# Optimization experiments

Hardware: AMD Instinct MI355X
Metric: run time of the kernel (lower is better)

Reference implementation:

```python
import jax, jax.numpy as jnp
import numpy as np

N, E = 50000, 800000
C_IN, C_OUT, HID = 64, 64, 64


def setup_inputs() -> dict:
    key = jax.random.key(0)
    ks = jax.random.split(key, 12)
    def rn(k, shape, scale=0.05):
        return jax.random.normal(k, shape, dtype=jnp.float32) * scale
    return dict(
        x=jax.random.normal(ks[0], (N, C_IN), dtype=jnp.float32),
        pos=jax.random.normal(ks[1], (N, 3), dtype=jnp.float32),
        edge_index=jax.random.randint(ks[2], (2, E), 0, N),
        W_in=rn(ks[3], (C_IN, C_IN)), b_in=jnp.zeros((C_IN,), jnp.float32),
        W_out=rn(ks[4], (C_OUT, C_OUT)), b_out=jnp.zeros((C_OUT,), jnp.float32),
        W_lin=rn(ks[5], (C_OUT, C_IN)),   # PointTransformerConv.lin (value), bias=False
        W_src=rn(ks[6], (C_OUT, C_IN)),   # lin_src, bias=False
        W_dst=rn(ks[7], (C_OUT, C_IN)),   # lin_dst, bias=False
        pos_w1=rn(ks[8], (HID, 3)), pos_b1=jnp.zeros((HID,), jnp.float32),
        pos_w2=rn(ks[9], (C_OUT, HID)), pos_b2=jnp.zeros((C_OUT,), jnp.float32),
        att_w1=rn(ks[10], (HID, C_OUT)), att_b1=jnp.zeros((HID,), jnp.float32),
        att_w2=rn(ks[11], (C_OUT, HID)), att_b2=jnp.zeros((C_OUT,), jnp.float32),
    )


def _mlp2(y, w1, b1, w2, b2):
    # MLP([a, 64, b], batch_norm=False): Linear->ReLU->Linear->ReLU
    y = jax.nn.relu(y @ w1.T + b1)
    return jax.nn.relu(y @ w2.T + b2)


def reference(x, pos, edge_index, W_in, b_in, W_out, b_out, W_lin, W_src, W_dst,
              pos_w1, pos_b1, pos_w2, pos_b2, att_w1, att_b1, att_w2, att_b2):
    n = x.shape[0]
    h = jax.nn.relu(x @ W_in.T + b_in)            # lin_in + relu, (N, C_in)
    v = h @ W_lin.T                                # value projection (N, C_out)
    k_src = h @ W_src.T                            # alpha_j source part
    q_dst = h @ W_dst.T                            # alpha_i dest part
    # PointTransformerConv adds self-loops by default
    loop = jnp.arange(n)
    src = jnp.concatenate([edge_index[0], loop])   # (E+N,)
    dst = jnp.concatenate([edge_index[1], loop])
    # per-edge positional encoding: pos_nn(pos_i - pos_j)
    delta = _mlp2(pos[dst] - pos[src], pos_w1, pos_b1, pos_w2, pos_b2)
    # per-edge attention logits: attn_nn(alpha_i - alpha_j), (E+N, C_out)
    alpha = _mlp2(q_dst[dst] - k_src[src], att_w1, att_b1, att_w2, att_b2)
    # per-destination-node channelwise softmax (self-loops ensure no empty segment)
    amax = jax.ops.segment_max(alpha, dst, num_segments=n)
    ex = jnp.exp(alpha - amax[dst])
    denom = jax.ops.segment_sum(ex, dst, num_segments=n)
    w = ex / (denom[dst] + 1e-16)
    # message = alpha * (x_j + delta); aggregate = sum over neighbors
    out = jax.ops.segment_sum(w * (v[src] + delta), dst, num_segments=n)
    return jax.nn.relu(out @ W_out.T + b_out)
```

## Files before the change

### kernel.cpp

```cpp
#include <hip/hip_runtime.h>
#include <math.h>

#define NN 50000
#define EE 800000
#define ET (EE + NN)
#define C  64
#define NBLK 49

typedef __attribute__((ext_vector_type(8))) _Float16 f16x8;
typedef __attribute__((ext_vector_type(4))) _Float16 f16x4;
typedef __attribute__((ext_vector_type(2))) _Float16 f16x2;
typedef __attribute__((ext_vector_type(4))) float f32x4;

__device__ __forceinline__ f16x2 pk2(float a, float b) {
  return __builtin_bit_cast(f16x2, __builtin_amdgcn_cvt_pkrtz(a, b));
}
__device__ __forceinline__ f16x4 pk4(float a, float b, float c, float d) {
  return __builtin_shufflevector(pk2(a, b), pk2(c, d), 0, 1, 2, 3);
}
__device__ __forceinline__ f16x8 pk8(const float* y) {
  const f16x4 lo = pk4(y[0], y[1], y[2], y[3]);
  const f16x4 hi = pk4(y[4], y[5], y[6], y[7]);
  return __builtin_shufflevector(lo, hi, 0, 1, 2, 3, 4, 5, 6, 7);
}

__device__ __forceinline__ f16x8 frag_ldh(const _Float16* base, int row,
                                          int kofs) {
  return *(const f16x8*)(base + row * 72 + kofs);
}

__device__ __forceinline__ void stage_w(_Float16* __restrict__ dst,
                                        const _Float16* __restrict__ src16,
                                        int tid) {
  const f16x8* src = (const f16x8*)(src16 + tid * 16);
  _Float16* d = dst + (tid >> 2) * 72 + (tid & 3) * 16;
  ((f16x8*)d)[0] = src[0];
  ((f16x8*)d)[1] = src[1];
}

__global__ __launch_bounds__(256) void prep_kernel(
    const float* __restrict__ W_in, const float* __restrict__ W_lin,
    const float* __restrict__ W_src, const float* __restrict__ W_dst,
    const float* __restrict__ att_w1, const float* __restrict__ att_w2,
    const float* __restrict__ pos_w2, const float* __restrict__ W_out,
    _Float16* __restrict__ w16) {
  const float* Ws[8] = {W_in, W_lin, W_src, W_dst, att_w1, att_w2, pos_w2, W_out};
  const float* src = Ws[blockIdx.x];
  _Float16* dst = w16 + blockIdx.x * 4096;
#pragma unroll
  for (int i = threadIdx.x * 4; i < 4096; i += 1024) {
    const float4 w = *(const float4*)(src + i);
    *(f16x4*)(dst + i) = pk4(w.x, w.y, w.z, w.w);
  }
}

__global__ __launch_bounds__(256) void scan_partial(const int* __restrict__ cnt,
                                                    int* __restrict__ bsum) {
  __shared__ int ws[4];
  const int t = threadIdx.x;
  const int base = blockIdx.x * 1024 + t * 4;
  int s = 0;
  if (base + 3 < NN) {
    const int4 v = *(const int4*)(cnt + base);
    s = v.x + v.y + v.z + v.w;
  } else {
#pragma unroll
    for (int i = 0; i < 4; ++i)
      if (base + i < NN) s += cnt[base + i];
  }
#pragma unroll
  for (int off = 32; off; off >>= 1) s += __shfl_down(s, off, 64);
  if ((t & 63) == 0) ws[t >> 6] = s;
  __syncthreads();
  if (t == 0) bsum[blockIdx.x] = ws[0] + ws[1] + ws[2] + ws[3];
}

__global__ __launch_bounds__(256) void scan_final(const int* __restrict__ cnt,
                                                  const int* __restrict__ bsum,
                                                  int* __restrict__ curs) {
  __shared__ int tsum[256];
  __shared__ int sblk[64];
  const int t = threadIdx.x;
  if (t < 64) {
    const int mine = (t < NBLK) ? bsum[t] : 0;
    int v = mine;
#pragma unroll
    for (int off = 1; off < 64; off <<= 1) {
      const int u = __shfl_up(v, off, 64);
      if (t >= off) v += u;
    }
    sblk[t] = v - mine;
  }
  const int base = blockIdx.x * 1024 + t * 4;
  int v[4] = {0, 0, 0, 0};
  if (base + 3 < NN) {
    const int4 x = *(const int4*)(cnt + base);
    v[0] = x.x; v[1] = x.y; v[2] = x.z; v[3] = x.w;
  } else {
#pragma unroll
    for (int i = 0; i < 4; ++i)
      if (base + i < NN) v[i] = cnt[base + i];
  }
  const int s = v[0] + v[1] + v[2] + v[3];
  tsum[t] = s;
  __syncthreads();
  for (int off = 1; off < 256; off <<= 1) {
    const int u = (t >= off) ? tsum[t - off] : 0;
    __syncthreads();
    tsum[t] += u;
    __syncthreads();
  }
  int ex = sblk[blockIdx.x] + tsum[t] - s;
#pragma unroll
  for (int i = 0; i < 4; ++i) {
    if (base + i < NN) curs[base + i] = ex;
    ex += v[i];
  }
}

__global__ void scatter_kernel(const int* __restrict__ ei,
                               int* __restrict__ curs, int2* __restrict__ srt) {
  const int e0 = (blockIdx.x * 256 + threadIdx.x) * 4;
  if (e0 >= ET) return;
  int s[4], d[4];
  if (e0 + 3 < EE) {
    const int4 sv = *(const int4*)(ei + e0);
    const int4 dv = *(const int4*)(ei + EE + e0);
    s[0] = sv.x; s[1] = sv.y; s[2] = sv.z; s[3] = sv.w;
    d[0] = dv.x; d[1] = dv.y; d[2] = dv.z; d[3] = dv.w;
  } else {
#pragma unroll
    for (int i = 0; i < 4; ++i) {
      const int e = e0 + i;
      if (e < EE) {
        s[i] = ei[e];
        d[i] = ei[EE + e];
      } else if (e < ET) {
        s[i] = d[i] = e - EE;
      } else {
        s[i] = d[i] = -1;
      }
    }
  }
#pragma unroll
  for (int i = 0; i < 4; ++i) {
    if (d[i] >= 0) {
      const int p = atomicAdd(&curs[d[i]], 1);
      srt[p] = make_int2(s[i], d[i]);
    }
  }
}

__global__ __launch_bounds__(256, 3) void node_proj(
    const float* __restrict__ x, const float* __restrict__ b_in,
    const _Float16* __restrict__ w16, const int* __restrict__ ei,
    int* __restrict__ cnt, _Float16* __restrict__ vh,
    _Float16* __restrict__ kh, _Float16* __restrict__ qh) {
  __shared__ __align__(16) _Float16 wlds[4 * 4608];
  __shared__ __align__(16) _Float16 hlds[4608];
  __shared__ float biasv[64];

  const int tid = threadIdx.x;
  const int nb = blockIdx.x * 64;
  const int l15 = tid & 15;
  const int quad = (tid >> 4) & 3;
  const int wband = tid >> 6;
  const int nloc = wband * 16 + l15;
  const int gn = nb + nloc;

  {
    const int stride = gridDim.x * 256;
    for (int e = blockIdx.x * 256 + tid; e < ET; e += stride) {
      const int d = (e < EE) ? ei[EE + e] : (e - EE);
      atomicAdd(&cnt[d], 1);
    }
  }

#pragma unroll
  for (int w = 0; w < 4; ++w) stage_w(wlds + w * 4608, w16 + w * 4096, tid);
  if (tid < 64) biasv[tid] = b_in[tid];

  f16x8 bfrag[2];
#pragma unroll
  for (int ks = 0; ks < 2; ++ks) {
    float y[8] = {0.f, 0.f, 0.f, 0.f, 0.f, 0.f, 0.f, 0.f};
    if (gn < NN) {
      const float4 a = *(const float4*)(x + (size_t)gn * 64 + ks * 32 + quad * 8);
      const float4 b = *(const float4*)(x + (size_t)gn * 64 + ks * 32 + quad * 8 + 4);
      y[0] = a.x; y[1] = a.y; y[2] = a.z; y[3] = a.w;
      y[4] = b.x; y[5] = b.y; y[6] = b.z; y[7] = b.w;
    }
    bfrag[ks] = pk8(y);
  }
  __syncthreads();

#pragma unroll
  for (int t = 0; t < 4; ++t) {
    f32x4 acc = {0.f, 0.f, 0.f, 0.f};
#pragma unroll
    for (int ks = 0; ks < 2; ++ks) {
      const f16x8 af = frag_ldh(wlds, t * 16 + l15, ks * 32 + quad * 8);
      acc = __builtin_amdgcn_mfma_f32_16x16x32_f16(af, bfrag[ks], acc, 0, 0, 0);
    }
    const int hb = t * 16 + quad * 4;
    *(f16x4*)(hlds + nloc * 72 + hb) =
        pk4(fmaxf(acc[0] + biasv[hb + 0], 0.f), fmaxf(acc[1] + biasv[hb + 1], 0.f),
            fmaxf(acc[2] + biasv[hb + 2], 0.f), fmaxf(acc[3] + biasv[hb + 3], 0.f));
  }
  __syncthreads();

  f16x8 hfrag[2];
#pragma unroll
  for (int ks = 0; ks < 2; ++ks)
    hfrag[ks] = frag_ldh(hlds, nloc, ks * 32 + quad * 8);

  _Float16* outs[3] = {vh, kh, qh};
#pragma unroll
  for (int p = 0; p < 3; ++p) {
    const _Float16* W = wlds + (p + 1) * 4608;
#pragma unroll
    for (int t = 0; t < 4; ++t) {
      f32x4 acc = {0.f, 0.f, 0.f, 0.f};
#pragma unroll
      for (int ks = 0; ks < 2; ++ks) {
        const f16x8 af = frag_ldh(W, t * 16 + l15, ks * 32 + quad * 8);
        acc = __builtin_amdgcn_mfma_f32_16x16x32_f16(af, hfrag[ks], acc, 0, 0, 0);
      }
      if (gn < NN) {
        *(f16x4*)(outs[p] + (size_t)gn * 64 + t * 16 + quad * 4) =
            pk4(acc[0], acc[1], acc[2], acc[3]);
      }
    }
  }
}

__global__ __launch_bounds__(256, 4) void edge_pass(
    const int2* __restrict__ srt, const float* __restrict__ pos,
    const _Float16* __restrict__ vh, const _Float16* __restrict__ kh,
    const _Float16* __restrict__ qh, const _Float16* __restrict__ w16,
    const float* __restrict__ att_b1, const float* __restrict__ att_b2,
    const float* __restrict__ pos_w1, const float* __restrict__ pos_b1,
    const float* __restrict__ pos_b2, float* __restrict__ num,
    float* __restrict__ den) {
  __shared__ __align__(16) _Float16 smem[18432];
  __shared__ __align__(16) float posw1T[3 * 64];
  __shared__ float b1s[64], b2s[64], pb1s[64], pb2s[64];
  __shared__ int dsts[64];

  _Float16* W1  = smem;
  _Float16* W2  = smem + 4608;
  _Float16* PW2 = smem + 9216;
  _Float16* h1  = smem + 13824;
  float2* pairb = (float2*)smem;

  const int tid = threadIdx.x;
  const int eb = blockIdx.x * 64;
  const int l15 = tid & 15;
  const int quad = (tid >> 4) & 3;
  const int wband = tid >> 6;
  const int eloc = wband * 16 + l15;

  int s_mine, d_mine;
  f16x8 bfrag[2];
  float dp0, dp1, dp2;
  {
    const int e = eb + eloc;
    int2 sd = make_int2(0, 0);
    int valid_d = -1;
    if (e < ET) {
      sd = srt[e];
      valid_d = sd.y;
    }
    s_mine = sd.x;
    d_mine = sd.y;
    if (quad == 0) dsts[eloc] = valid_d;
#pragma unroll
    for (int ks = 0; ks < 2; ++ks) {
      const f16x8 qv =
          *(const f16x8*)(qh + (size_t)d_mine * 64 + ks * 32 + quad * 8);
      const f16x8 kv =
          *(const f16x8*)(kh + (size_t)s_mine * 64 + ks * 32 + quad * 8);
      bfrag[ks] = qv - kv;
    }
    dp0 = pos[(size_t)d_mine * 3 + 0] - pos[(size_t)s_mine * 3 + 0];
    dp1 = pos[(size_t)d_mine * 3 + 1] - pos[(size_t)s_mine * 3 + 1];
    dp2 = pos[(size_t)d_mine * 3 + 2] - pos[(size_t)s_mine * 3 + 2];
  }

  stage_w(W1, w16 + 4 * 4096, tid);
  stage_w(W2, w16 + 5 * 4096, tid);
  stage_w(PW2, w16 + 6 * 4096, tid);
  if (tid < 64) {
    b1s[tid] = att_b1[tid];
    b2s[tid] = att_b2[tid];
    pb1s[tid] = pos_b1[tid];
    pb2s[tid] = pos_b2[tid];
    posw1T[0 * 64 + tid] = pos_w1[tid * 3 + 0];
    posw1T[1 * 64 + tid] = pos_w1[tid * 3 + 1];
    posw1T[2 * 64 + tid] = pos_w1[tid * 3 + 2];
  }
  __syncthreads();

#pragma unroll
  for (int t = 0; t < 4; ++t) {
    f32x4 acc = {0.f, 0.f, 0.f, 0.f};
#pragma unroll
    for (int ks = 0; ks < 2; ++ks) {
      const f16x8 af = frag_ldh(W1, t * 16 + l15, ks * 32 + quad * 8);
      acc = __builtin_amdgcn_mfma_f32_16x16x32_f16(af, bfrag[ks], acc, 0, 0, 0);
    }
    const int hb = t * 16 + quad * 4;
    *(f16x4*)(h1 + eloc * 72 + hb) =
        pk4(fmaxf(acc[0] + b1s[hb + 0], 0.f), fmaxf(acc[1] + b1s[hb + 1], 0.f),
            fmaxf(acc[2] + b1s[hb + 2], 0.f), fmaxf(acc[3] + b1s[hb + 3], 0.f));
  }

  f16x8 hpfrag[2];
#pragma unroll
  for (int ks = 0; ks < 2; ++ks) {
    float hv[8];
#pragma unroll
    for (int j = 0; j < 8; ++j) {
      const int i = ks * 32 + quad * 8 + j;
      float a = pb1s[i];
      a = fmaf(dp0, posw1T[i], a);
      a = fmaf(dp1, posw1T[64 + i], a);
      a = fmaf(dp2, posw1T[128 + i], a);
      hv[j] = fmaxf(a, 0.f);
    }
    hpfrag[ks] = pk8(hv);
  }
  __syncthreads();

  float ex[16], del[16];
  {
    f16x8 hfrag[2];
#pragma unroll
    for (int ks = 0; ks < 2; ++ks)
      hfrag[ks] = frag_ldh(h1, eloc, ks * 32 + quad * 8);
#pragma unroll
    for (int t = 0; t < 4; ++t) {
      f32x4 acc = {0.f, 0.f, 0.f, 0.f};
#pragma unroll
      for (int ks = 0; ks < 2; ++ks) {
        const f16x8 af = frag_ldh(W2, t * 16 + l15, ks * 32 + quad * 8);
        acc = __builtin_amdgcn_mfma_f32_16x16x32_f16(af, hfrag[ks], acc, 0, 0, 0);
      }
      const int ob = t * 16 + quad * 4;
#pragma unroll
      for (int r = 0; r < 4; ++r)
        ex[t * 4 + r] = __expf(fmaxf(acc[r] + b2s[ob + r], 0.f));
    }
  }
#pragma unroll
  for (int t = 0; t < 4; ++t) {
    f32x4 acc = {0.f, 0.f, 0.f, 0.f};
#pragma unroll
    for (int ks = 0; ks < 2; ++ks) {
      const f16x8 af = frag_ldh(PW2, t * 16 + l15, ks * 32 + quad * 8);
      acc = __builtin_amdgcn_mfma_f32_16x16x32_f16(af, hpfrag[ks], acc, 0, 0, 0);
    }
    const int ob = t * 16 + quad * 4;
#pragma unroll
    for (int r = 0; r < 4; ++r)
      del[t * 4 + r] = fmaxf(acc[r] + pb2s[ob + r], 0.f);
  }
  float vr[16];
#pragma unroll
  for (int t = 0; t < 4; ++t) {
    const f16x4 v4 = *(const f16x4*)(vh + (size_t)s_mine * 64 + t * 16 + quad * 4);
    vr[t * 4 + 0] = (float)v4[0];
    vr[t * 4 + 1] = (float)v4[1];
    vr[t * 4 + 2] = (float)v4[2];
    vr[t * 4 + 3] = (float)v4[3];
  }
  __syncthreads();

#pragma unroll
  for (int t = 0; t < 4; ++t) {
#pragma unroll
    for (int r = 0; r < 4; ++r) {
      const int o = t * 16 + quad * 4 + r;
      const int sl = (eloc + 2 * o) & 63;
      const float e_ = ex[t * 4 + r];
      pairb[o * 65 + sl] = make_float2(e_ * (vr[t * 4 + r] + del[t * 4 + r]), e_);
    }
  }
  __syncthreads();

  {
    const int c = tid & 63;
    const int r = tid >> 6;
    float am = 0.f, ae = 0.f;
    int cur = -1;
#pragma unroll 1
    for (int t2 = 0; t2 < 16; ++t2) {
      const int el = r * 16 + t2;
      const int d = dsts[el];
      if (d != cur) {
        if (cur >= 0) {
          unsafeAtomicAdd(num + (size_t)cur * 64 + c, am);
          unsafeAtomicAdd(den + (size_t)cur * 64 + c, ae);
        }
        cur = d;
        am = 0.f;
        ae = 0.f;
      }
      if (d >= 0) {
        const float2 pe = pairb[c * 65 + ((el + 2 * c) & 63)];
        am += pe.x;
        ae += pe.y;
      }
    }
    if (cur >= 0) {
      unsafeAtomicAdd(num + (size_t)cur * 64 + c, am);
      unsafeAtomicAdd(den + (size_t)cur * 64 + c, ae);
    }
  }
}

__global__ __launch_bounds__(256, 4) void out_proj(
    const float* __restrict__ num, const float* __restrict__ den,
    const _Float16* __restrict__ w16, const float* __restrict__ b_out,
    float* __restrict__ out) {
  __shared__ __align__(16) _Float16 wlds[4608];
  __shared__ float biasv[64];

  const int tid = threadIdx.x;
  const int nb = blockIdx.x * 64;
  const int l15 = tid & 15;
  const int quad = (tid >> 4) & 3;
  const int wband = tid >> 6;
  const int gn = nb + wband * 16 + l15;

  stage_w(wlds, w16 + 7 * 4096, tid);
  if (tid < 64) biasv[tid] = b_out[tid];

  f16x8 bfrag[2];
#pragma unroll
  for (int ks = 0; ks < 2; ++ks) {
    float y[8] = {0.f, 0.f, 0.f, 0.f, 0.f, 0.f, 0.f, 0.f};
    if (gn < NN) {
      const size_t base = (size_t)gn * 64 + ks * 32 + quad * 8;
      const float4 n0 = *(const float4*)(num + base);
      const float4 n1 = *(const float4*)(num + base + 4);
      const float4 d0 = *(const float4*)(den + base);
      const float4 d1 = *(const float4*)(den + base + 4);
      y[0] = n0.x / (d0.x + 1e-16f); y[1] = n0.y / (d0.y + 1e-16f);
      y[2] = n0.z / (d0.z + 1e-16f); y[3] = n0.w / (d0.w + 1e-16f);
      y[4] = n1.x / (d1.x + 1e-16f); y[5] = n1.y / (d1.y + 1e-16f);
      y[6] = n1.z / (d1.z + 1e-16f); y[7] = n1.w / (d1.w + 1e-16f);
    }
    bfrag[ks] = pk8(y);
  }
  __syncthreads();

#pragma unroll
  for (int t = 0; t < 4; ++t) {
    f32x4 acc = {0.f, 0.f, 0.f, 0.f};
#pragma unroll
    for (int ks = 0; ks < 2; ++ks) {
      const f16x8 af = frag_ldh(wlds, t * 16 + l15, ks * 32 + quad * 8);
      acc = __builtin_amdgcn_mfma_f32_16x16x32_f16(af, bfrag[ks], acc, 0, 0, 0);
    }
    if (gn < NN) {
      const int ob = t * 16 + quad * 4;
      float4 r;
      r.x = fmaxf(acc[0] + biasv[ob + 0], 0.f);
      r.y = fmaxf(acc[1] + biasv[ob + 1], 0.f);
      r.z = fmaxf(acc[2] + biasv[ob + 2], 0.f);
      r.w = fmaxf(acc[3] + biasv[ob + 3], 0.f);
      *(float4*)(out + (size_t)gn * 64 + ob) = r;
    }
  }
}

extern "C" void kernel_launch(void* const* d_in, const int* in_sizes, int n_in,
                              void* d_out, int out_size, void* d_ws,
                              size_t ws_size, hipStream_t stream) {
  const float* x      = (const float*)d_in[0];
  const float* pos    = (const float*)d_in[1];
  const int*   ei     = (const int*)d_in[2];
  const float* W_in   = (const float*)d_in[3];
  const float* b_in   = (const float*)d_in[4];
  const float* W_out  = (const float*)d_in[5];
  const float* b_out  = (const float*)d_in[6];
  const float* W_lin  = (const float*)d_in[7];
  const float* W_src  = (const float*)d_in[8];
  const float* W_dst  = (const float*)d_in[9];
  const float* pos_w1 = (const float*)d_in[10];
  const float* pos_b1 = (const float*)d_in[11];
  const float* pos_w2 = (const float*)d_in[12];
  const float* pos_b2 = (const float*)d_in[13];
  const float* att_w1 = (const float*)d_in[14];
  const float* att_b1 = (const float*)d_in[15];
  const float* att_w2 = (const float*)d_in[16];
  const float* att_b2 = (const float*)d_in[17];

  float* ws = (float*)d_ws;
  const size_t NC = (size_t)NN * C;
  float* num = ws;
  float* den = ws + NC;
  _Float16* vh = (_Float16*)(ws + 2 * NC);
  _Float16* kh = vh + NC;
  _Float16* qh = kh + NC;
  _Float16* w16 = qh + NC;
  int* ib    = (int*)(w16 + 8 * 4096);
  int* cnt   = ib;
  int* curs  = ib + NN;
  int* bsum  = ib + 2 * NN;
  int2* srt  = (int2*)(((uintptr_t)(bsum + NBLK) + 15) & ~(uintptr_t)15);

  hipMemsetAsync(num, 0, 2 * NC * sizeof(float), stream);
  hipMemsetAsync(cnt, 0, NN * sizeof(int), stream);

  const dim3 blk(256);
  prep_kernel<<<dim3(8), blk, 0, stream>>>(W_in, W_lin, W_src, W_dst, att_w1,
                                           att_w2, pos_w2, W_out, w16);
  node_proj<<<dim3((NN + 63) / 64), blk, 0, stream>>>(x, b_in, w16, ei, cnt, vh,
                                                      kh, qh);
  scan_partial<<<dim3(NBLK), blk, 0, stream>>>(cnt, bsum);
  scan_final<<<dim3(NBLK), blk, 0, stream>>>(cnt, bsum, curs);
  scatter_kernel<<<dim3((ET + 1023) / 1024), blk, 0, stream>>>(ei, curs, srt);
  edge_pass<<<dim3((ET + 63) / 64), blk, 0, stream>>>(
      srt, pos, vh, kh, qh, w16, att_b1, att_b2, pos_w1, pos_b1, pos_b2, num,
      den);
  out_proj<<<dim3((NN + 63) / 64), blk, 0, stream>>>(num, den, w16, b_out,
                                                     (float*)d_out);
}
```

Before: 315.3 us.

## Shard degree counters eight ways and fold memsets into existing kernels

Edge-degree counting and scatter cursors are split into 8 shards selected by chunk index, spreading atomics on hot destination counters across separate arrays. The scans now sum and offset across shards so the stable per-shard cursors still give a valid CSR layout. The two hipMemsetAsync calls are replaced with zeroing inside prep_kernel (counters) and extra blocks in scan_partial (num/den accumulators), removing separate memset launches. The cost is 8x more counter memory, more reads in the scans, and extra work in scan_partial.

```diff
diff --git a/kernel.cpp b/kernel.cpp
--- a/kernel.cpp
+++ b/kernel.cpp
@@ -6,6 +6,8 @@
 #define ET (EE + NN)
 #define C  64
 #define NBLK 49
+#define NCHUNK 831
+#define ZBLK 463
 
 typedef __attribute__((ext_vector_type(8))) _Float16 f16x8;
 typedef __attribute__((ext_vector_type(4))) _Float16 f16x4;
@@ -43,7 +45,7 @@
     const float* __restrict__ W_src, const float* __restrict__ W_dst,
     const float* __restrict__ att_w1, const float* __restrict__ att_w2,
     const float* __restrict__ pos_w2, const float* __restrict__ W_out,
-    _Float16* __restrict__ w16) {
+    _Float16* __restrict__ w16, int* __restrict__ cnt2) {
   const float* Ws[8] = {W_in, W_lin, W_src, W_dst, att_w1, att_w2, pos_w2, W_out};
   const float* src = Ws[blockIdx.x];
   _Float16* dst = w16 + blockIdx.x * 4096;
@@ -52,21 +54,39 @@
     const float4 w = *(const float4*)(src + i);
     *(f16x4*)(dst + i) = pk4(w.x, w.y, w.z, w.w);
   }
-}
-
-__global__ __launch_bounds__(256) void scan_partial(const int* __restrict__ cnt,
-                                                    int* __restrict__ bsum) {
+  int4* cz = (int4*)(cnt2 + blockIdx.x * NN);
+#pragma unroll 1
+  for (int i = threadIdx.x; i < NN / 4; i += 256) cz[i] = make_int4(0, 0, 0, 0);
+}
+
+__global__ __launch_bounds__(256) void scan_partial(const int* __restrict__ cnt2,
+                                                    int* __restrict__ bsum,
+                                                    float* __restrict__ zeroreg) {
+  const int t = threadIdx.x;
+  if (blockIdx.x >= NBLK) {
+    const int zb = blockIdx.x - NBLK;
+    float4* dst = (float4*)zeroreg;
+    const int total4 = 2 * NN * 64 / 4;
+    const float4 z = make_float4(0.f, 0.f, 0.f, 0.f);
+#pragma unroll 1
+    for (int i = zb * 256 + t; i < total4; i += ZBLK * 256) dst[i] = z;
+    return;
+  }
   __shared__ int ws[4];
-  const int t = threadIdx.x;
   const int base = blockIdx.x * 1024 + t * 4;
   int s = 0;
   if (base + 3 < NN) {
-    const int4 v = *(const int4*)(cnt + base);
-    s = v.x + v.y + v.z + v.w;
+#pragma unroll
+    for (int sh = 0; sh < 8; ++sh) {
+      const int4 v = *(const int4*)(cnt2 + sh * NN + base);
+      s += v.x + v.y + v.z + v.w;
+    }
   } else {
 #pragma unroll
     for (int i = 0; i < 4; ++i)
-      if (base + i < NN) s += cnt[base + i];
+      if (base + i < NN)
+#pragma unroll
+        for (int sh = 0; sh < 8; ++sh) s += cnt2[sh * NN + base + i];
   }
 #pragma unroll
   for (int off = 32; off; off >>= 1) s += __shfl_down(s, off, 64);
@@ -75,9 +95,9 @@
   if (t == 0) bsum[blockIdx.x] = ws[0] + ws[1] + ws[2] + ws[3];
 }
 
-__global__ __launch_bounds__(256) void scan_final(const int* __restrict__ cnt,
+__global__ __launch_bounds__(256) void scan_final(const int* __restrict__ cnt2,
                                                   const int* __restrict__ bsum,
-                                                  int* __restrict__ curs) {
+                                                  int* __restrict__ curs2) {
   __shared__ int tsum[256];
   __shared__ int sblk[64];
   const int t = threadIdx.x;
@@ -92,14 +112,24 @@
     sblk[t] = v - mine;
   }
   const int base = blockIdx.x * 1024 + t * 4;
+  int c2[8][4];
   int v[4] = {0, 0, 0, 0};
   if (base + 3 < NN) {
-    const int4 x = *(const int4*)(cnt + base);
-    v[0] = x.x; v[1] = x.y; v[2] = x.z; v[3] = x.w;
+#pragma unroll
+    for (int sh = 0; sh < 8; ++sh) {
+      const int4 x = *(const int4*)(cnt2 + sh * NN + base);
+      c2[sh][0] = x.x; c2[sh][1] = x.y; c2[sh][2] = x.z; c2[sh][3] = x.w;
+      v[0] += x.x; v[1] += x.y; v[2] += x.z; v[3] += x.w;
+    }
   } else {
 #pragma unroll
-    for (int i = 0; i < 4; ++i)
-      if (base + i < NN) v[i] = cnt[base + i];
+    for (int sh = 0; sh < 8; ++sh)
+#pragma unroll
+      for (int i = 0; i < 4; ++i) {
+        const int c = (base + i < NN) ? cnt2[sh * NN + base + i] : 0;
+        c2[sh][i] = c;
+        v[i] += c;
+      }
   }
   const int s = v[0] + v[1] + v[2] + v[3];
   tsum[t] = s;
@@ -111,16 +141,36 @@
     __syncthreads();
   }
   int ex = sblk[blockIdx.x] + tsum[t] - s;
+  int offs[8][4];
 #pragma unroll
   for (int i = 0; i < 4; ++i) {
-    if (base + i < NN) curs[base + i] = ex;
+    int run = ex;
+#pragma unroll
+    for (int sh = 0; sh < 8; ++sh) {
+      offs[sh][i] = run;
+      run += c2[sh][i];
+    }
     ex += v[i];
   }
+  if (base + 3 < NN) {
+#pragma unroll
+    for (int sh = 0; sh < 8; ++sh)
+      *(int4*)(curs2 + sh * NN + base) =
+          make_int4(offs[sh][0], offs[sh][1], offs[sh][2], offs[sh][3]);
+  } else {
+#pragma unroll
+    for (int sh = 0; sh < 8; ++sh)
+#pragma unroll
+      for (int i = 0; i < 4; ++i)
+        if (base + i < NN) curs2[sh * NN + base + i] = offs[sh][i];
+  }
 }
 
 __global__ void scatter_kernel(const int* __restrict__ ei,
-                               int* __restrict__ curs, int2* __restrict__ srt) {
-  const int e0 = (blockIdx.x * 256 + threadIdx.x) * 4;
+                               int* __restrict__ curs2, int2* __restrict__ srt) {
+  const int chunk = blockIdx.x;
+  int* cs = curs2 + (chunk & 7) * NN;
+  const int e0 = chunk * 1024 + threadIdx.x * 4;
   if (e0 >= ET) return;
   int s[4], d[4];
   if (e0 + 3 < EE) {
@@ -145,7 +195,7 @@
 #pragma unroll
   for (int i = 0; i < 4; ++i) {
     if (d[i] >= 0) {
-      const int p = atomicAdd(&curs[d[i]], 1);
+      const int p = atomicAdd(&cs[d[i]], 1);
       srt[p] = make_int2(s[i], d[i]);
     }
   }
@@ -154,7 +204,7 @@
 __global__ __launch_bounds__(256, 3) void node_proj(
     const float* __restrict__ x, const float* __restrict__ b_in,
     const _Float16* __restrict__ w16, const int* __restrict__ ei,
-    int* __restrict__ cnt, _Float16* __restrict__ vh,
+    int* __restrict__ cnt2, _Float16* __restrict__ vh,
     _Float16* __restrict__ kh, _Float16* __restrict__ qh) {
   __shared__ __align__(16) _Float16 wlds[4 * 4608];
   __shared__ __align__(16) _Float16 hlds[4608];
@@ -168,11 +218,25 @@
   const int nloc = wband * 16 + l15;
   const int gn = nb + nloc;
 
-  {
-    const int stride = gridDim.x * 256;
-    for (int e = blockIdx.x * 256 + tid; e < ET; e += stride) {
-      const int d = (e < EE) ? ei[EE + e] : (e - EE);
-      atomicAdd(&cnt[d], 1);
+#pragma unroll 1
+  for (int chunk = blockIdx.x; chunk < NCHUNK; chunk += gridDim.x) {
+    int* cs = cnt2 + (chunk & 7) * NN;
+    const int e0 = chunk * 1024 + tid * 4;
+    if (e0 < ET) {
+      int d[4];
+      if (e0 + 3 < EE) {
+        const int4 dv = *(const int4*)(ei + EE + e0);
+        d[0] = dv.x; d[1] = dv.y; d[2] = dv.z; d[3] = dv.w;
+      } else {
+#pragma unroll
+        for (int i = 0; i < 4; ++i) {
+          const int e = e0 + i;
+          d[i] = (e < EE) ? ei[EE + e] : ((e < ET) ? e - EE : -1);
+        }
+      }
+#pragma unroll
+      for (int i = 0; i < 4; ++i)
+        if (d[i] >= 0) atomicAdd(&cs[d[i]], 1);
     }
   }
 
@@ -505,23 +569,20 @@
   _Float16* kh = vh + NC;
   _Float16* qh = kh + NC;
   _Float16* w16 = qh + NC;
-  int* ib    = (int*)(w16 + 8 * 4096);
-  int* cnt   = ib;
-  int* curs  = ib + NN;
-  int* bsum  = ib + 2 * NN;
-  int2* srt  = (int2*)(((uintptr_t)(bsum + NBLK) + 15) & ~(uintptr_t)15);
-
-  hipMemsetAsync(num, 0, 2 * NC * sizeof(float), stream);
-  hipMemsetAsync(cnt, 0, NN * sizeof(int), stream);
+  int* ib     = (int*)(w16 + 8 * 4096);
+  int* cnt2   = ib;
+  int* curs2  = ib + 8 * NN;
+  int* bsum   = ib + 16 * NN;
+  int2* srt   = (int2*)(((uintptr_t)(bsum + NBLK) + 15) & ~(uintptr_t)15);
 
   const dim3 blk(256);
   prep_kernel<<<dim3(8), blk, 0, stream>>>(W_in, W_lin, W_src, W_dst, att_w1,
-                                           att_w2, pos_w2, W_out, w16);
-  node_proj<<<dim3((NN + 63) / 64), blk, 0, stream>>>(x, b_in, w16, ei, cnt, vh,
-                                                      kh, qh);
-  scan_partial<<<dim3(NBLK), blk, 0, stream>>>(cnt, bsum);
-  scan_final<<<dim3(NBLK), blk, 0, stream>>>(cnt, bsum, curs);
-  scatter_kernel<<<dim3((ET + 1023) / 1024), blk, 0, stream>>>(ei, curs, srt);
+                                           att_w2, pos_w2, W_out, w16, cnt2);
+  node_proj<<<dim3((NN + 63) / 64), blk, 0, stream>>>(x, b_in, w16, ei, cnt2,
+                                                      vh, kh, qh);
+  scan_partial<<<dim3(NBLK + ZBLK), blk, 0, stream>>>(cnt2, bsum, num);
+  scan_final<<<dim3(NBLK), blk, 0, stream>>>(cnt2, bsum, curs2);
+  scatter_kernel<<<dim3(NCHUNK), blk, 0, stream>>>(ei, curs2, srt);
   edge_pass<<<dim3((ET + 63) / 64), blk, 0, stream>>>(
       srt, pos, vh, kh, qh, w16, att_b1, att_b2, pos_w1, pos_b1, pos_b2, num,
       den);
```

Result: faster. 307.3 us (-2.5%).
